# Kernel tuning notes

Measured on AMD Instinct MI355X. Metric: run time of the kernel, lower is better.

## Reference

```python
import jax, jax.numpy as jnp
import numpy as np

HIDDEN = 1024
HEADS = 16
HEAD_DIM = HIDDEN // HEADS
SCALE = 1.0 / np.sqrt(HEAD_DIM)
B, S = 2, 2048


def setup_inputs() -> dict:
    key = jax.random.key(0)
    ks = jax.random.split(key, 12)
    std = 1.0 / np.sqrt(HIDDEN)
    inp = {
        "x": jax.random.normal(ks[0], (B, S, HIDDEN), jnp.float32),
        "pos_emb": jax.random.normal(ks[1], (B, S, HIDDEN), jnp.float32),
        "mask": jnp.ones((B, S, S), jnp.int32),
        "wq": jax.random.normal(ks[2], (HIDDEN, HIDDEN), jnp.float32) * std,
        "bq": jnp.zeros((HIDDEN,), jnp.float32),
        "wk": jax.random.normal(ks[3], (HIDDEN, HIDDEN), jnp.float32) * std,
        "bk": jnp.zeros((HIDDEN,), jnp.float32),
        "wv": jax.random.normal(ks[4], (HIDDEN, HIDDEN), jnp.float32) * std,
        "bv": jnp.zeros((HIDDEN,), jnp.float32),
        "wo": jax.random.normal(ks[5], (HIDDEN, HIDDEN), jnp.float32) * std,
        "bo": jnp.zeros((HIDDEN,), jnp.float32),
        "w_pos": jax.random.normal(ks[6], (HEADS, HIDDEN), jnp.float32) * std,
    }
    return inp


def reference(x, pos_emb, mask, wq, bq, wk, bk, wv, bv, wo, bo, w_pos):
    b, s, d = x.shape
    # QKV projections (torch Linear: y = x @ W.T + b), split into heads -> (b, h, s, hd)
    q = (x @ wq.T + bq).reshape(b, s, HEADS, HEAD_DIM).transpose(0, 2, 1, 3)
    k = (x @ wk.T + bk).reshape(b, s, HEADS, HEAD_DIM).transpose(0, 2, 1, 3)
    v = (x @ wv.T + bv).reshape(b, s, HEADS, HEAD_DIM).transpose(0, 2, 1, 3)
    # learned positional bias: (b, s, heads) -> (b, heads, s), broadcast over query axis
    pos_bias = (pos_emb @ w_pos.T).transpose(0, 2, 1)  # (b, h, s_key)
    scores = jnp.einsum("bhqd,bhkd->bhqk", q, k) * SCALE
    scores = scores + pos_bias[:, :, None, :]
    scores = jnp.where(mask[:, None, :, :] == 0, -jnp.inf, scores)
    attn = jax.nn.softmax(scores.astype(jnp.float32), axis=-1).astype(q.dtype)
    # dropout p=0.0 -> identity
    out = jnp.einsum("bhqk,bhkd->bhqd", attn, v)
    out = out.transpose(0, 2, 1, 3).reshape(b, s, d)
    return out @ wo.T + bo
```

## Files before the change

### kernel.cpp

```cpp
#include <hip/hip_runtime.h>
#include <stdint.h>

typedef unsigned short u16;
typedef unsigned int u32;
typedef unsigned long long u64;
typedef __attribute__((ext_vector_type(8))) short short8;
typedef __attribute__((ext_vector_type(4))) float f32x4;

#define MFMA16(a,b,c) __builtin_amdgcn_mfma_f32_16x16x32_bf16((a),(b),(c),0,0,0)

__device__ __forceinline__ u16 f2bf(float f){
  u32 u = __builtin_bit_cast(u32, f);
  u32 r = u + 0x7FFFu + ((u >> 16) & 1u);
  return (u16)(r >> 16);
}

__device__ __forceinline__ void gload16(const void* g, void* l){
  __builtin_amdgcn_global_load_lds((__attribute__((address_space(1))) void*)(uintptr_t)g,
                                   (__attribute__((address_space(3))) void*)l, 16, 0, 0);
}

__global__ __launch_bounds__(256) void k_prep(const float* __restrict__ x,
    const float* __restrict__ wq, const float* __restrict__ wk,
    const float* __restrict__ wv, const float* __restrict__ wo,
    u16* __restrict__ xb, u16* __restrict__ wqb, u16* __restrict__ wkb,
    u16* __restrict__ wvb, u16* __restrict__ wob){
  for (int j = blockIdx.x*blockDim.x + threadIdx.x; j < 2097152; j += gridDim.x*blockDim.x){
    const float* src; u16* dst; int off;
    if (j < 1048576){ src = x; dst = xb; off = j; }
    else {
      int r = (j - 1048576) >> 18; off = (j - 1048576) & 262143;
      src = (r==0)?wq:(r==1)?wk:(r==2)?wv:wo;
      dst = (r==0)?wqb:(r==1)?wkb:(r==2)?wvb:wob;
    }
    float4 v = ((const float4*)src)[off];
    ushort4 o;
    o.x = f2bf(v.x); o.y = f2bf(v.y); o.z = f2bf(v.z); o.w = f2bf(v.w);
    ((ushort4*)dst)[off] = o;
  }
}

__global__ __launch_bounds__(256) void k_posb(const float* __restrict__ pos,
    const float* __restrict__ wpos, float* __restrict__ posb){
  int row = blockIdx.x*4 + (threadIdx.x >> 6);
  int lane = threadIdx.x & 63;
  const float* pr = pos + (size_t)row*1024;
  float pv[16];
  #pragma unroll
  for (int t=0;t<4;t++){
    float4 v = ((const float4*)pr)[lane + 64*t];
    pv[4*t+0]=v.x; pv[4*t+1]=v.y; pv[4*t+2]=v.z; pv[4*t+3]=v.w;
  }
  int b = row >> 11, s = row & 2047;
  for (int h=0; h<16; h++){
    const float* wr = wpos + h*1024;
    float acc = 0.f;
    #pragma unroll
    for (int t=0;t<4;t++){
      float4 w = ((const float4*)wr)[lane + 64*t];
      acc += pv[4*t+0]*w.x + pv[4*t+1]*w.y + pv[4*t+2]*w.z + pv[4*t+3]*w.w;
    }
    #pragma unroll
    for (int m=1;m<64;m<<=1) acc += __shfl_xor(acc, m);
    if (lane == 0) posb[(b*16 + h)*2048 + s] = acc * 1.44269504f;
  }
}

__global__ __launch_bounds__(256) void k_mask(const int* __restrict__ mask, u64* __restrict__ pm){
  int wi = (blockIdx.x*blockDim.x + threadIdx.x) >> 6;
  int lane = threadIdx.x & 63;
  int nw = (gridDim.x*blockDim.x) >> 6;
  for (int w = wi; w < 131072; w += nw){
    int v = mask[(size_t)w*64 + lane];
    u64 bits = __ballot(v != 0);
    if (lane == 0) pm[w] = bits;
  }
}

__global__ __launch_bounds__(256) void k_qkv(const u16* __restrict__ xb,
    const u16* __restrict__ wqb, const u16* __restrict__ wkb, const u16* __restrict__ wvb,
    const float* __restrict__ bq, const float* __restrict__ bk, const float* __restrict__ bv,
    u16* __restrict__ Q, u16* __restrict__ K, u16* __restrict__ V){
  __shared__ __align__(16) u16 As[128*32];
  __shared__ __align__(16) u16 Bs[128*32];
  const int bx = blockIdx.x, by = blockIdx.y;
  const int tid = threadIdx.x, wid = tid >> 6, lane = tid & 63;
  const int wsel = by >> 3;
  const u16* W = (wsel==0) ? wqb : (wsel==1 ? wkb : wvb);
  const float* bias = (wsel==0) ? bq : (wsel==1 ? bk : bv);
  u16* dst = (wsel==0) ? Q : (wsel==1 ? K : V);
  const int m0 = bx*128, n0 = (by & 7)*128;
  const int wm = wid >> 1, wn = wid & 1;
  const int g8 = (lane >> 4)*8;

  f32x4 acc[4][4];
  f32x4 z4 = {0.f,0.f,0.f,0.f};
  #pragma unroll
  for (int mf=0;mf<4;mf++)
    #pragma unroll
    for (int nf=0;nf<4;nf++) acc[mf][nf] = z4;

  for (int kt=0; kt<32; kt++){
    #pragma unroll
    for (int jj=0;jj<2;jj++){
      int sp = wid*2 + jj;
      int p = sp*64 + lane;
      int row = p >> 2, c4 = p & 3;
      gload16(xb + (size_t)(m0+row)*1024 + kt*32 + c4*8, &As[sp*512]);
      gload16(W  + (size_t)(n0+row)*1024 + kt*32 + c4*8, &Bs[sp*512]);
    }
    __syncthreads();
    short8 a[4], b[4];
    #pragma unroll
    for (int mf=0;mf<4;mf++) a[mf] = *(const short8*)&As[(wm*64 + mf*16 + (lane&15))*32 + g8];
    #pragma unroll
    for (int nf=0;nf<4;nf++) b[nf] = *(const short8*)&Bs[(wn*64 + nf*16 + (lane&15))*32 + g8];
    #pragma unroll
    for (int mf=0;mf<4;mf++)
      #pragma unroll
      for (int nf=0;nf<4;nf++) acc[mf][nf] = MFMA16(a[mf], b[nf], acc[mf][nf]);
    __syncthreads();
  }

  #pragma unroll
  for (int nf=0;nf<4;nf++){
    int nloc = n0 + wn*64 + nf*16 + (lane & 15);
    float bb = bias[nloc];
    int h = nloc >> 6, d = nloc & 63;
    #pragma unroll
    for (int mf=0;mf<4;mf++)
      #pragma unroll
      for (int i=0;i<4;i++){
        int m = m0 + wm*64 + mf*16 + (lane>>4)*4 + i;
        int bt = m >> 11, s = m & 2047;
        u16 val = f2bf(acc[mf][nf][i] + bb);
        if (wsel == 2)
          dst[((size_t)((bt*16 + h)*64 + d))*2048 + s] = val;
        else
          dst[((size_t)((bt*16 + h)*2048 + s))*64 + d] = val;
      }
  }
}

__global__ __launch_bounds__(256) void k_attn(const u16* __restrict__ Qg, const u16* __restrict__ Kg,
    const u16* __restrict__ Vtg, const float* __restrict__ posb, const u64* __restrict__ pmask,
    u16* __restrict__ AO){
  __shared__ __align__(16) u16 Ks[64*64];
  __shared__ __align__(16) u16 Vts[64*64];
  __shared__ __align__(16) u16 Ps[4*16*64];
  const int bid = blockIdx.x;
  const int bh = bid >> 5;
  const int qt = bid & 31;
  const int b_ = bh >> 4;
  const int h_ = bh & 15;
  const int tid = threadIdx.x, wid = tid >> 6, lane = tid & 63;
  const int g = lane >> 4, c = lane & 15;
  const int q0w = qt*64 + wid*16;
  const float SC = 0.125f * 1.44269504f;

  short8 qf0, qf1;
  {
    const u16* qp = Qg + ((size_t)(bh*2048 + q0w + c))*64 + g*8;
    qf0 = *(const short8*)qp;
    qf1 = *(const short8*)(qp + 32);
  }
  f32x4 Oa[4];
  f32x4 z4 = {0.f,0.f,0.f,0.f};
  #pragma unroll
  for (int i=0;i<4;i++) Oa[i] = z4;
  float mi[4], li[4];
  #pragma unroll
  for (int i=0;i<4;i++){ mi[i] = -1e30f; li[i] = 0.f; }

  u16* Pw = Ps + wid*1024;

  for (int kt=0; kt<32; kt++){
    if (wid < 2){
      #pragma unroll
      for (int jj=0;jj<4;jj++){
        int sx = wid*4 + jj;
        int p = sx*64 + lane;
        int key = p >> 3, o16 = p & 7;
        gload16(Kg + ((size_t)(bh*2048 + kt*64 + key))*64 + (o16 ^ (key&7))*8, &Ks[sx*512]);
      }
    } else {
      #pragma unroll
      for (int jj=0;jj<4;jj++){
        int sv = (wid-2)*4 + jj;
        int p = sv*64 + lane;
        int d = p >> 3, o16 = p & 7;
        gload16(Vtg + ((size_t)(bh*64 + d))*2048 + kt*64 + (o16 ^ (d&7))*8, &Vts[sv*512]);
      }
    }
    __syncthreads();

    f32x4 sc[4];
    #pragma unroll
    for (int nf=0;nf<4;nf++) sc[nf] = z4;
    #pragma unroll
    for (int ks=0;ks<2;ks++){
      short8 qf = ks ? qf1 : qf0;
      #pragma unroll
      for (int nf=0;nf<4;nf++){
        int key = nf*16 + c;
        unsigned off = (unsigned)(key*128 + ks*64 + g*16) ^ (unsigned)((key&7)<<4);
        short8 kb = *(const short8*)((const char*)Ks + off);
        sc[nf] = MFMA16(qf, kb, sc[nf]);
      }
    }

    float pb[4];
    #pragma unroll
    for (int nf=0;nf<4;nf++) pb[nf] = posb[bh*2048 + kt*64 + nf*16 + c];
    u64 mw[4];
    #pragma unroll
    for (int i=0;i<4;i++) mw[i] = pmask[((size_t)(b_*2048 + q0w + g*4 + i))*32 + kt];

    float pv_[4][4], rowmax[4];
    #pragma unroll
    for (int i=0;i<4;i++){
      u64 m = mw[i];
      #pragma unroll
      for (int nf=0;nf<4;nf++) pv_[nf][i] = sc[nf][i]*SC + pb[nf];
      if (m != ~0ull){
        #pragma unroll
        for (int nf=0;nf<4;nf++)
          if (!((m >> (nf*16 + c)) & 1ull)) pv_[nf][i] = -1e30f;
      }
      float t = fmaxf(fmaxf(pv_[0][i], pv_[1][i]), fmaxf(pv_[2][i], pv_[3][i]));
      t = fmaxf(t, __shfl_xor(t, 1));
      t = fmaxf(t, __shfl_xor(t, 2));
      t = fmaxf(t, __shfl_xor(t, 4));
      t = fmaxf(t, __shfl_xor(t, 8));
      rowmax[i] = t;
    }
    float need = rowmax[0] - mi[0];
    need = fmaxf(need, rowmax[1] - mi[1]);
    need = fmaxf(need, rowmax[2] - mi[2]);
    need = fmaxf(need, rowmax[3] - mi[3]);
    if (__any(need > 8.0f)){
      #pragma unroll
      for (int i=0;i<4;i++){
        float mn = fmaxf(mi[i], rowmax[i]);
        float al = __builtin_amdgcn_exp2f(mi[i] - mn);
        mi[i] = mn;
        li[i] *= al;
        #pragma unroll
        for (int db=0;db<4;db++) Oa[db][i] *= al;
      }
    }
    #pragma unroll
    for (int i=0;i<4;i++){
      float rs = 0.f;
      #pragma unroll
      for (int nf=0;nf<4;nf++){
        float e = __builtin_amdgcn_exp2f(pv_[nf][i] - mi[i]);
        pv_[nf][i] = e;
        rs += e;
      }
      rs += __shfl_xor(rs, 1);
      rs += __shfl_xor(rs, 2);
      rs += __shfl_xor(rs, 4);
      rs += __shfl_xor(rs, 8);
      li[i] += rs;
    }

    #pragma unroll
    for (int i=0;i<4;i++){
      int qr = g*4 + i;
      #pragma unroll
      for (int nf=0;nf<4;nf++){
        unsigned off = (unsigned)(qr*128 + (nf*16 + c)*2) ^ (unsigned)((qr&7)<<4);
        *(u16*)((char*)Pw + off) = f2bf(pv_[nf][i]);
      }
    }
    __syncthreads();

    #pragma unroll
    for (int ks=0;ks<2;ks++){
      unsigned aoff = (unsigned)(c*128 + ks*64 + g*16) ^ (unsigned)((c&7)<<4);
      short8 pa = *(const short8*)((const char*)Pw + aoff);
      #pragma unroll
      for (int db=0;db<4;db++){
        int d = db*16 + c;
        unsigned boff = (unsigned)(d*128 + ks*64 + g*16) ^ (unsigned)((d&7)<<4);
        short8 vb = *(const short8*)((const char*)Vts + boff);
        Oa[db] = MFMA16(pa, vb, Oa[db]);
      }
    }
    __syncthreads();
  }

  #pragma unroll
  for (int i=0;i<4;i++){
    float inv = 1.0f / li[i];
    int q = q0w + g*4 + i;
    size_t base = ((size_t)(b_*2048 + q))*1024 + h_*64;
    #pragma unroll
    for (int db=0;db<4;db++)
      AO[base + db*16 + c] = f2bf(Oa[db][i] * inv);
  }
}

__global__ __launch_bounds__(256) void k_out(const u16* __restrict__ A, const u16* __restrict__ W,
    const float* __restrict__ bo, float* __restrict__ out){
  __shared__ __align__(16) u16 As[128*32];
  __shared__ __align__(16) u16 Bs[128*32];
  const int bx = blockIdx.x, by = blockIdx.y;
  const int tid = threadIdx.x, wid = tid >> 6, lane = tid & 63;
  const int m0 = bx*128, n0 = by*128;
  const int wm = wid >> 1, wn = wid & 1;
  const int g8 = (lane >> 4)*8;

  f32x4 acc[4][4];
  f32x4 z4 = {0.f,0.f,0.f,0.f};
  #pragma unroll
  for (int mf=0;mf<4;mf++)
    #pragma unroll
    for (int nf=0;nf<4;nf++) acc[mf][nf] = z4;

  for (int kt=0; kt<32; kt++){
    #pragma unroll
    for (int jj=0;jj<2;jj++){
      int sp = wid*2 + jj;
      int p = sp*64 + lane;
      int row = p >> 2, c4 = p & 3;
      gload16(A + (size_t)(m0+row)*1024 + kt*32 + c4*8, &As[sp*512]);
      gload16(W + (size_t)(n0+row)*1024 + kt*32 + c4*8, &Bs[sp*512]);
    }
    __syncthreads();
    short8 a[4], b[4];
    #pragma unroll
    for (int mf=0;mf<4;mf++) a[mf] = *(const short8*)&As[(wm*64 + mf*16 + (lane&15))*32 + g8];
    #pragma unroll
    for (int nf=0;nf<4;nf++) b[nf] = *(const short8*)&Bs[(wn*64 + nf*16 + (lane&15))*32 + g8];
    #pragma unroll
    for (int mf=0;mf<4;mf++)
      #pragma unroll
      for (int nf=0;nf<4;nf++) acc[mf][nf] = MFMA16(a[mf], b[nf], acc[mf][nf]);
    __syncthreads();
  }

  #pragma unroll
  for (int nf=0;nf<4;nf++){
    int n = n0 + wn*64 + nf*16 + (lane & 15);
    float bb = bo[n];
    #pragma unroll
    for (int mf=0;mf<4;mf++)
      #pragma unroll
      for (int i=0;i<4;i++){
        int m = m0 + wm*64 + mf*16 + (lane>>4)*4 + i;
        out[(size_t)m*1024 + n] = acc[mf][nf][i] + bb;
      }
  }
}

extern "C" void kernel_launch(void* const* d_in, const int* in_sizes, int n_in,
                              void* d_out, int out_size, void* d_ws, size_t ws_size,
                              hipStream_t stream){
  const float* x    = (const float*)d_in[0];
  const float* pos  = (const float*)d_in[1];
  const int*   mask = (const int*)d_in[2];
  const float* wq   = (const float*)d_in[3];
  const float* bq   = (const float*)d_in[4];
  const float* wk   = (const float*)d_in[5];
  const float* bk   = (const float*)d_in[6];
  const float* wv   = (const float*)d_in[7];
  const float* bv   = (const float*)d_in[8];
  const float* wo   = (const float*)d_in[9];
  const float* bo   = (const float*)d_in[10];
  const float* wpos = (const float*)d_in[11];
  float* out = (float*)d_out;

  char* ws = (char*)d_ws;
  u16* xb   = (u16*)(ws);
  u16* wqb  = (u16*)(ws + ((size_t)8  << 20));
  u16* wkb  = (u16*)(ws + ((size_t)10 << 20));
  u16* wvb  = (u16*)(ws + ((size_t)12 << 20));
  u16* wob  = (u16*)(ws + ((size_t)14 << 20));
  u16* Qb   = (u16*)(ws + ((size_t)16 << 20));
  u16* Kb   = (u16*)(ws + ((size_t)24 << 20));
  u16* Vtb  = (u16*)(ws + ((size_t)32 << 20));
  u16* AO   = (u16*)(ws + ((size_t)40 << 20));
  float* posb = (float*)(ws + ((size_t)48 << 20));
  u64* pm   = (u64*)(ws + ((size_t)49 << 20));

  k_prep<<<dim3(2048), dim3(256), 0, stream>>>(x, wq, wk, wv, wo, xb, wqb, wkb, wvb, wob);
  k_posb<<<dim3(1024), dim3(256), 0, stream>>>(pos, wpos, posb);
  k_mask<<<dim3(1024), dim3(256), 0, stream>>>(mask, pm);
  k_qkv<<<dim3(32,24), dim3(256), 0, stream>>>(xb, wqb, wkb, wvb, bq, bk, bv, Qb, Kb, Vtb);
  k_attn<<<dim3(1024), dim3(256), 0, stream>>>(Qb, Kb, Vtb, posb, pm, AO);
  k_out<<<dim3(32,8), dim3(256), 0, stream>>>(AO, wob, bo, out);
}
```

Baseline: 366.2 us.

## Double-buffer LDS tiles in all GEMM/attention kernels and defer softmax row-sum reduction

Adds two-stage LDS buffering to the QKV, attention and output kernels so the next tile's global->LDS load is issued before the current tile's MFMAs, aiming to hide memory latency. In attention, the per-tile row-sum shuffles are moved to a single reduction at the end, the row-max shuffles run only when a rescale is needed, and the sync between the P write and the PV read is dropped since each wave uses its own P region. Blocks are also remapped so that neighbouring block IDs land on different heads. The changes double LDS use, which may lower occupancy. It is unclear whether the loop-end barrier alone orders the async next-tile load correctly, and when no rescale occurs the lane-local max is used, which may not bound the row exactly.

Measured after the change: 330.3 us. 1.11x faster.

```diff
diff --git a/kernel.cpp b/kernel.cpp
--- a/kernel.cpp
+++ b/kernel.cpp
@@ -81,8 +81,8 @@
     const u16* __restrict__ wqb, const u16* __restrict__ wkb, const u16* __restrict__ wvb,
     const float* __restrict__ bq, const float* __restrict__ bk, const float* __restrict__ bv,
     u16* __restrict__ Q, u16* __restrict__ K, u16* __restrict__ V){
-  __shared__ __align__(16) u16 As[128*32];
-  __shared__ __align__(16) u16 Bs[128*32];
+  __shared__ __align__(16) u16 As[2][128*32];
+  __shared__ __align__(16) u16 Bs[2][128*32];
   const int bx = blockIdx.x, by = blockIdx.y;
   const int tid = threadIdx.x, wid = tid >> 6, lane = tid & 63;
   const int wsel = by >> 3;
@@ -93,28 +93,34 @@
   const int wm = wid >> 1, wn = wid & 1;
   const int g8 = (lane >> 4)*8;
 
-  f32x4 acc[4][4];
-  f32x4 z4 = {0.f,0.f,0.f,0.f};
-  #pragma unroll
-  for (int mf=0;mf<4;mf++)
-    #pragma unroll
-    for (int nf=0;nf<4;nf++) acc[mf][nf] = z4;
-
-  for (int kt=0; kt<32; kt++){
+  auto stage = [&](int kt, int buf){
     #pragma unroll
     for (int jj=0;jj<2;jj++){
       int sp = wid*2 + jj;
       int p = sp*64 + lane;
       int row = p >> 2, c4 = p & 3;
-      gload16(xb + (size_t)(m0+row)*1024 + kt*32 + c4*8, &As[sp*512]);
-      gload16(W  + (size_t)(n0+row)*1024 + kt*32 + c4*8, &Bs[sp*512]);
-    }
-    __syncthreads();
+      gload16(xb + (size_t)(m0+row)*1024 + kt*32 + c4*8, &As[buf][sp*512]);
+      gload16(W  + (size_t)(n0+row)*1024 + kt*32 + c4*8, &Bs[buf][sp*512]);
+    }
+  };
+
+  f32x4 acc[4][4];
+  f32x4 z4 = {0.f,0.f,0.f,0.f};
+  #pragma unroll
+  for (int mf=0;mf<4;mf++)
+    #pragma unroll
+    for (int nf=0;nf<4;nf++) acc[mf][nf] = z4;
+
+  stage(0, 0);
+  __syncthreads();
+  for (int kt=0; kt<32; kt++){
+    int cur = kt & 1;
+    if (kt+1 < 32) stage(kt+1, cur^1);
     short8 a[4], b[4];
     #pragma unroll
-    for (int mf=0;mf<4;mf++) a[mf] = *(const short8*)&As[(wm*64 + mf*16 + (lane&15))*32 + g8];
-    #pragma unroll
-    for (int nf=0;nf<4;nf++) b[nf] = *(const short8*)&Bs[(wn*64 + nf*16 + (lane&15))*32 + g8];
+    for (int mf=0;mf<4;mf++) a[mf] = *(const short8*)&As[cur][(wm*64 + mf*16 + (lane&15))*32 + g8];
+    #pragma unroll
+    for (int nf=0;nf<4;nf++) b[nf] = *(const short8*)&Bs[cur][(wn*64 + nf*16 + (lane&15))*32 + g8];
     #pragma unroll
     for (int mf=0;mf<4;mf++)
       #pragma unroll
@@ -145,10 +151,11 @@
 __global__ __launch_bounds__(256) void k_attn(const u16* __restrict__ Qg, const u16* __restrict__ Kg,
     const u16* __restrict__ Vtg, const float* __restrict__ posb, const u64* __restrict__ pmask,
     u16* __restrict__ AO){
-  __shared__ __align__(16) u16 Ks[64*64];
-  __shared__ __align__(16) u16 Vts[64*64];
+  __shared__ __align__(16) u16 Ks[2][64*64];
+  __shared__ __align__(16) u16 Vts[2][64*64];
   __shared__ __align__(16) u16 Ps[4*16*64];
-  const int bid = blockIdx.x;
+  const int bid0 = blockIdx.x;
+  const int bid = (bid0 & 7)*128 + (bid0 >> 3);
   const int bh = bid >> 5;
   const int qt = bid & 31;
   const int b_ = bh >> 4;
@@ -174,14 +181,14 @@
 
   u16* Pw = Ps + wid*1024;
 
-  for (int kt=0; kt<32; kt++){
+  auto stage = [&](int kt, int buf){
     if (wid < 2){
       #pragma unroll
       for (int jj=0;jj<4;jj++){
         int sx = wid*4 + jj;
         int p = sx*64 + lane;
         int key = p >> 3, o16 = p & 7;
-        gload16(Kg + ((size_t)(bh*2048 + kt*64 + key))*64 + (o16 ^ (key&7))*8, &Ks[sx*512]);
+        gload16(Kg + ((size_t)(bh*2048 + kt*64 + key))*64 + (o16 ^ (key&7))*8, &Ks[buf][sx*512]);
       }
     } else {
       #pragma unroll
@@ -189,10 +196,17 @@
         int sv = (wid-2)*4 + jj;
         int p = sv*64 + lane;
         int d = p >> 3, o16 = p & 7;
-        gload16(Vtg + ((size_t)(bh*64 + d))*2048 + kt*64 + (o16 ^ (d&7))*8, &Vts[sv*512]);
-      }
-    }
-    __syncthreads();
+        gload16(Vtg + ((size_t)(bh*64 + d))*2048 + kt*64 + (o16 ^ (d&7))*8, &Vts[buf][sv*512]);
+      }
+    }
+  };
+
+  stage(0, 0);
+  __syncthreads();
+
+  for (int kt=0; kt<32; kt++){
+    const int cur = kt & 1;
+    if (kt+1 < 32) stage(kt+1, cur^1);
 
     f32x4 sc[4];
     #pragma unroll
@@ -204,7 +218,7 @@
       for (int nf=0;nf<4;nf++){
         int key = nf*16 + c;
         unsigned off = (unsigned)(key*128 + ks*64 + g*16) ^ (unsigned)((key&7)<<4);
-        short8 kb = *(const short8*)((const char*)Ks + off);
+        short8 kb = *(const short8*)((const char*)&Ks[cur][0] + off);
         sc[nf] = MFMA16(qf, kb, sc[nf]);
       }
     }
@@ -216,7 +230,7 @@
     #pragma unroll
     for (int i=0;i<4;i++) mw[i] = pmask[((size_t)(b_*2048 + q0w + g*4 + i))*32 + kt];
 
-    float pv_[4][4], rowmax[4];
+    float pv_[4][4], lmax[4];
     #pragma unroll
     for (int i=0;i<4;i++){
       u64 m = mw[i];
@@ -227,21 +241,19 @@
         for (int nf=0;nf<4;nf++)
           if (!((m >> (nf*16 + c)) & 1ull)) pv_[nf][i] = -1e30f;
       }
-      float t = fmaxf(fmaxf(pv_[0][i], pv_[1][i]), fmaxf(pv_[2][i], pv_[3][i]));
-      t = fmaxf(t, __shfl_xor(t, 1));
-      t = fmaxf(t, __shfl_xor(t, 2));
-      t = fmaxf(t, __shfl_xor(t, 4));
-      t = fmaxf(t, __shfl_xor(t, 8));
-      rowmax[i] = t;
-    }
-    float need = rowmax[0] - mi[0];
-    need = fmaxf(need, rowmax[1] - mi[1]);
-    need = fmaxf(need, rowmax[2] - mi[2]);
-    need = fmaxf(need, rowmax[3] - mi[3]);
+      lmax[i] = fmaxf(fmaxf(pv_[0][i], pv_[1][i]), fmaxf(pv_[2][i], pv_[3][i]));
+    }
+    float need = fmaxf(fmaxf(lmax[0]-mi[0], lmax[1]-mi[1]),
+                       fmaxf(lmax[2]-mi[2], lmax[3]-mi[3]));
     if (__any(need > 8.0f)){
       #pragma unroll
       for (int i=0;i<4;i++){
-        float mn = fmaxf(mi[i], rowmax[i]);
+        float t = lmax[i];
+        t = fmaxf(t, __shfl_xor(t, 1));
+        t = fmaxf(t, __shfl_xor(t, 2));
+        t = fmaxf(t, __shfl_xor(t, 4));
+        t = fmaxf(t, __shfl_xor(t, 8));
+        float mn = fmaxf(mi[i], t);
         float al = __builtin_amdgcn_exp2f(mi[i] - mn);
         mi[i] = mn;
         li[i] *= al;
@@ -258,10 +270,6 @@
         pv_[nf][i] = e;
         rs += e;
       }
-      rs += __shfl_xor(rs, 1);
-      rs += __shfl_xor(rs, 2);
-      rs += __shfl_xor(rs, 4);
-      rs += __shfl_xor(rs, 8);
       li[i] += rs;
     }
 
@@ -274,7 +282,6 @@
         *(u16*)((char*)Pw + off) = f2bf(pv_[nf][i]);
       }
     }
-    __syncthreads();
 
     #pragma unroll
     for (int ks=0;ks<2;ks++){
@@ -284,7 +291,7 @@
       for (int db=0;db<4;db++){
         int d = db*16 + c;
         unsigned boff = (unsigned)(d*128 + ks*64 + g*16) ^ (unsigned)((d&7)<<4);
-        short8 vb = *(const short8*)((const char*)Vts + boff);
+        short8 vb = *(const short8*)((const char*)&Vts[cur][0] + boff);
         Oa[db] = MFMA16(pa, vb, Oa[db]);
       }
     }
@@ -293,7 +300,12 @@
 
   #pragma unroll
   for (int i=0;i<4;i++){
-    float inv = 1.0f / li[i];
+    float s = li[i];
+    s += __shfl_xor(s, 1);
+    s += __shfl_xor(s, 2);
+    s += __shfl_xor(s, 4);
+    s += __shfl_xor(s, 8);
+    float inv = 1.0f / s;
     int q = q0w + g*4 + i;
     size_t base = ((size_t)(b_*2048 + q))*1024 + h_*64;
     #pragma unroll
@@ -304,36 +316,42 @@
 
 __global__ __launch_bounds__(256) void k_out(const u16* __restrict__ A, const u16* __restrict__ W,
     const float* __restrict__ bo, float* __restrict__ out){
-  __shared__ __align__(16) u16 As[128*32];
-  __shared__ __align__(16) u16 Bs[128*32];
+  __shared__ __align__(16) u16 As[2][128*32];
+  __shared__ __align__(16) u16 Bs[2][128*32];
   const int bx = blockIdx.x, by = blockIdx.y;
   const int tid = threadIdx.x, wid = tid >> 6, lane = tid & 63;
   const int m0 = bx*128, n0 = by*128;
   const int wm = wid >> 1, wn = wid & 1;
   const int g8 = (lane >> 4)*8;
 
-  f32x4 acc[4][4];
-  f32x4 z4 = {0.f,0.f,0.f,0.f};
-  #pragma unroll
-  for (int mf=0;mf<4;mf++)
-    #pragma unroll
-    for (int nf=0;nf<4;nf++) acc[mf][nf] = z4;
-
-  for (int kt=0; kt<32; kt++){
+  auto stage = [&](int kt, int buf){
     #pragma unroll
     for (int jj=0;jj<2;jj++){
       int sp = wid*2 + jj;
       int p = sp*64 + lane;
       int row = p >> 2, c4 = p & 3;
-      gload16(A + (size_t)(m0+row)*1024 + kt*32 + c4*8, &As[sp*512]);
-      gload16(W + (size_t)(n0+row)*1024 + kt*32 + c4*8, &Bs[sp*512]);
-    }
-    __syncthreads();
+      gload16(A + (size_t)(m0+row)*1024 + kt*32 + c4*8, &As[buf][sp*512]);
+      gload16(W + (size_t)(n0+row)*1024 + kt*32 + c4*8, &Bs[buf][sp*512]);
+    }
+  };
+
+  f32x4 acc[4][4];
+  f32x4 z4 = {0.f,0.f,0.f,0.f};
+  #pragma unroll
+  for (int mf=0;mf<4;mf++)
+    #pragma unroll
+    for (int nf=0;nf<4;nf++) acc[mf][nf] = z4;
+
+  stage(0, 0);
+  __syncthreads();
+  for (int kt=0; kt<32; kt++){
+    int cur = kt & 1;
+    if (kt+1 < 32) stage(kt+1, cur^1);
     short8 a[4], b[4];
     #pragma unroll
-    for (int mf=0;mf<4;mf++) a[mf] = *(const short8*)&As[(wm*64 + mf*16 + (lane&15))*32 + g8];
-    #pragma unroll
-    for (int nf=0;nf<4;nf++) b[nf] = *(const short8*)&Bs[(wn*64 + nf*16 + (lane&15))*32 + g8];
+    for (int mf=0;mf<4;mf++) a[mf] = *(const short8*)&As[cur][(wm*64 + mf*16 + (lane&15))*32 + g8];
+    #pragma unroll
+    for (int nf=0;nf<4;nf++) b[nf] = *(const short8*)&Bs[cur][(wn*64 + nf*16 + (lane&15))*32 + g8];
     #pragma unroll
     for (int mf=0;mf<4;mf++)
       #pragma unroll
```
